# Performance work log

Measured on AMD Instinct MI355X. Metric: run time of the kernel, lower is better.

The kernel has to match this reference:

```python
import jax, jax.numpy as jnp
import numpy as np

K_MSG = 1024   # message length k (rows of G)
N_CODE = 2048  # codeword length n (cols of G)
B = 32768      # number of message blocks


def setup_inputs() -> dict:
    key = jax.random.key(0)
    kb, kg = jax.random.split(key)
    b = jax.random.randint(kb, (B, K_MSG), 0, 2, dtype=jnp.int32)
    G = jax.random.randint(kg, (K_MSG, N_CODE), 0, 2, dtype=jnp.int32)
    return {"b": b, "G": G}


def reference(b, G):
    # GF(2) linear block encode: c = (b @ G) mod 2
    # b: [num_blocks, k] bits (0/1), G: [k, n] generator matrix (0/1)
    b2 = b.astype(jnp.int32)
    G2 = G.astype(jnp.int32)
    c = jnp.mod(jnp.matmul(b2, G2), 2)  # [num_blocks, n]
    return c.astype(jnp.int32)
```

## Files before the change

kernel.cpp:

```cpp
#include <hip/hip_runtime.h>
#include <stdint.h>

typedef unsigned long long u64;
typedef unsigned int u32;
typedef u32 v4u __attribute__((ext_vector_type(4)));

#define K_MSG   1024
#define N_CODE  2048
#define NB      32768
#define KW      16
#define ROWS_TILE 256
#define COLS_PER_BLOCK 256

__global__ void pack_b_kernel(const int* __restrict__ b, u64* __restrict__ bp,
                              int nwords) {
    const int lane  = threadIdx.x & 63;
    const int wave  = blockIdx.x * (blockDim.x >> 6) + (threadIdx.x >> 6);
    const int nwave = gridDim.x * (blockDim.x >> 6);
    for (int word = wave; word < nwords; word += nwave) {
        int v = b[(size_t)word * 64 + lane];
        u64 m = __ballot((v & 1) != 0);
        if (lane == 0) bp[word] = m;
    }
}

__global__ void pack_g_kernel(const int* __restrict__ G, u64* __restrict__ gp) {
    const int lane = threadIdx.x & 63;
    const int wave = blockIdx.x * (blockDim.x >> 6) + (threadIdx.x >> 6);
    const int w    = wave >> 5;
    const int jb   = wave & 31;
    const int j    = jb * 64 + lane;
    u64 word = 0;
#pragma unroll 16
    for (int t = 0; t < 64; ++t) {
        int v = G[(size_t)(w * 64 + t) * N_CODE + j];
        word |= (u64)(v & 1) << t;
    }
    gp[(size_t)w * N_CODE + j] = word;
}

__global__ __launch_bounds__(256, 4) void encode_main(const u64* __restrict__ bp,
                                                      const u64* __restrict__ gp,
                                                      int* __restrict__ out) {
    __shared__ u32 rows[ROWS_TILE * 32];

    const int tid = threadIdx.x;
    const int j   = blockIdx.x * COLS_PER_BLOCK + tid;
    const int r0  = blockIdx.y * ROWS_TILE;

    u32 g[32];
#pragma unroll
    for (int w = 0; w < KW; ++w) {
        u64 v = gp[(size_t)w * N_CODE + j];
        g[2 * w]     = (u32)v;
        g[2 * w + 1] = (u32)(v >> 32);
    }

    {
        const v4u* __restrict__ src = (const v4u*)(bp + ((size_t)r0 << 4));
        v4u* dst = (v4u*)rows;
#pragma unroll
        for (int i = 0; i < 8; ++i)
            dst[tid + COLS_PER_BLOCK * i] = src[tid + COLS_PER_BLOCK * i];
    }
    __syncthreads();

    int* __restrict__ op = out + (size_t)r0 * N_CODE + j;

#pragma unroll 2
    for (int r = 0; r < ROWS_TILE; ++r) {
        const u32* rw = &rows[r * 32];
        u32 a0 = 0, a1 = 0, a2 = 0, a3 = 0;
#pragma unroll
        for (int i = 0; i < 8; ++i) {
            a0 ^= rw[i]      & g[i];
            a1 ^= rw[8 + i]  & g[8 + i];
            a2 ^= rw[16 + i] & g[16 + i];
            a3 ^= rw[24 + i] & g[24 + i];
        }
        u32 acc = (a0 ^ a1) ^ (a2 ^ a3);
        op[(size_t)r * N_CODE] = (int)(__popc(acc) & 1);
    }
}

__global__ void encode_naive(const int* __restrict__ b, const int* __restrict__ G,
                             int* __restrict__ out) {
    size_t idx = (size_t)blockIdx.x * blockDim.x + threadIdx.x;
    size_t total = (size_t)NB * N_CODE;
    if (idx >= total) return;
    int i = (int)(idx / N_CODE);
    int j = (int)(idx % N_CODE);
    int acc = 0;
    for (int k = 0; k < K_MSG; ++k)
        acc ^= b[(size_t)i * K_MSG + k] & G[(size_t)k * N_CODE + j];
    out[idx] = acc & 1;
}

extern "C" void kernel_launch(void* const* d_in, const int* in_sizes, int n_in,
                              void* d_out, int out_size, void* d_ws, size_t ws_size,
                              hipStream_t stream) {
    const int* b = (const int*)d_in[0];
    const int* G = (const int*)d_in[1];
    int* out = (int*)d_out;

    const size_t bp_bytes = (size_t)NB * KW * sizeof(u64);
    const size_t gp_bytes = (size_t)N_CODE * KW * sizeof(u64);

    if (ws_size < bp_bytes + gp_bytes) {
        size_t total = (size_t)NB * N_CODE;
        encode_naive<<<(unsigned)((total + 255) / 256), 256, 0, stream>>>(b, G, out);
        return;
    }

    u64* bp = (u64*)d_ws;
    u64* gp = (u64*)((char*)d_ws + bp_bytes);

    pack_b_kernel<<<2048, 256, 0, stream>>>(b, bp, NB * KW);
    pack_g_kernel<<<128, 256, 0, stream>>>(G, gp);

    dim3 grid(N_CODE / COLS_PER_BLOCK, NB / ROWS_TILE);
    encode_main<<<grid, 256, 0, stream>>>(bp, gp, out);
}
```

Measured before the change: 159.5 us.

## Replace bit-packed XOR/popcount encode with int8 MFMA GEMM

Replaces the 64-bit bit-packing and per-thread AND/XOR/popcount loop with an int8 GEMM on the matrix cores. The message matrix is packed to one byte per bit, and G is transposed to byte form. A double-buffered LDS-tiled kernel then accumulates with mfma_i32_32x32x32_i8 and takes the result mod 2. This moves the bulk arithmetic onto MFMA units, but the packed operands become 8x larger (32 MB for b instead of 4 MB), and the output stores from MFMA fragments are less coalesced.

```diff
diff --git a/kernel.cpp b/kernel.cpp
--- a/kernel.cpp
+++ b/kernel.cpp
@@ -1,85 +1,116 @@
 #include <hip/hip_runtime.h>
 #include <stdint.h>
 
-typedef unsigned long long u64;
 typedef unsigned int u32;
-typedef u32 v4u __attribute__((ext_vector_type(4)));
+typedef int v4i  __attribute__((ext_vector_type(4)));
+typedef int v16i __attribute__((ext_vector_type(16)));
 
 #define K_MSG   1024
 #define N_CODE  2048
 #define NB      32768
-#define KW      16
-#define ROWS_TILE 256
-#define COLS_PER_BLOCK 256
+#define BM 128
+#define BN 128
+#define BK 64
+#define BKP 80
 
-__global__ void pack_b_kernel(const int* __restrict__ b, u64* __restrict__ bp,
-                              int nwords) {
-    const int lane  = threadIdx.x & 63;
-    const int wave  = blockIdx.x * (blockDim.x >> 6) + (threadIdx.x >> 6);
-    const int nwave = gridDim.x * (blockDim.x >> 6);
-    for (int word = wave; word < nwords; word += nwave) {
-        int v = b[(size_t)word * 64 + lane];
-        u64 m = __ballot((v & 1) != 0);
-        if (lane == 0) bp[word] = m;
+__global__ void pack_bi8(const int* __restrict__ b, u32* __restrict__ bi8) {
+    const int nthr = gridDim.x * blockDim.x;
+    int idx = blockIdx.x * blockDim.x + threadIdx.x;
+    const int ndw = NB * K_MSG / 4;
+    for (; idx < ndw; idx += nthr) {
+        int4 v = *(const int4*)(b + (size_t)idx * 4);
+        bi8[idx] = (u32)(v.x & 1) | ((u32)(v.y & 1) << 8) |
+                   ((u32)(v.z & 1) << 16) | ((u32)(v.w & 1) << 24);
     }
 }
 
-__global__ void pack_g_kernel(const int* __restrict__ G, u64* __restrict__ gp) {
-    const int lane = threadIdx.x & 63;
-    const int wave = blockIdx.x * (blockDim.x >> 6) + (threadIdx.x >> 6);
-    const int w    = wave >> 5;
-    const int jb   = wave & 31;
-    const int j    = jb * 64 + lane;
-    u64 word = 0;
-#pragma unroll 16
-    for (int t = 0; t < 64; ++t) {
-        int v = G[(size_t)(w * 64 + t) * N_CODE + j];
-        word |= (u64)(v & 1) << t;
+__global__ void pack_gT8(const int* __restrict__ G, u32* __restrict__ gt8) {
+    int idx = blockIdx.x * blockDim.x + threadIdx.x;
+    const int j  = idx & (N_CODE - 1);
+    const int kq = idx >> 11;
+    u32 p = 0;
+#pragma unroll
+    for (int i = 0; i < 4; ++i) {
+        int v = G[(size_t)(kq * 4 + i) * N_CODE + j];
+        p |= (u32)(v & 1) << (8 * i);
     }
-    gp[(size_t)w * N_CODE + j] = word;
+    gt8[(size_t)j * (K_MSG / 4) + kq] = p;
 }
 
-__global__ __launch_bounds__(256, 4) void encode_main(const u64* __restrict__ bp,
-                                                      const u64* __restrict__ gp,
-                                                      int* __restrict__ out) {
-    __shared__ u32 rows[ROWS_TILE * 32];
+__global__ __launch_bounds__(256) void gemm_i8(const char* __restrict__ bi8,
+                                               const char* __restrict__ gt8,
+                                               int* __restrict__ out) {
+    __shared__ __align__(16) char As[2][BM][BKP];
+    __shared__ __align__(16) char Bs[2][BN][BKP];
 
-    const int tid = threadIdx.x;
-    const int j   = blockIdx.x * COLS_PER_BLOCK + tid;
-    const int r0  = blockIdx.y * ROWS_TILE;
+    const int t    = threadIdx.x;
+    const int m0   = blockIdx.y * BM;
+    const int n0   = blockIdx.x * BN;
+    const int srow = t & 127;
+    const int kh   = t >> 7;
+    const int w    = t >> 6, lane = t & 63, hi = lane >> 5, lr = lane & 31;
+    const int wm   = w >> 1, wn = w & 1;
 
-    u32 g[32];
-#pragma unroll
-    for (int w = 0; w < KW; ++w) {
-        u64 v = gp[(size_t)w * N_CODE + j];
-        g[2 * w]     = (u32)v;
-        g[2 * w + 1] = (u32)(v >> 32);
-    }
+    v16i acc[2][2] = {};
+
+    const char* aseg = bi8 + (size_t)(m0 + srow) * K_MSG + kh * 32;
+    const char* bseg = gt8 + (size_t)(n0 + srow) * K_MSG + kh * 32;
 
     {
-        const v4u* __restrict__ src = (const v4u*)(bp + ((size_t)r0 << 4));
-        v4u* dst = (v4u*)rows;
-#pragma unroll
-        for (int i = 0; i < 8; ++i)
-            dst[tid + COLS_PER_BLOCK * i] = src[tid + COLS_PER_BLOCK * i];
+        uint4 a0 = *(const uint4*)(aseg);
+        uint4 a1 = *(const uint4*)(aseg + 16);
+        uint4 b0 = *(const uint4*)(bseg);
+        uint4 b1 = *(const uint4*)(bseg + 16);
+        *(uint4*)&As[0][srow][kh * 32]      = a0;
+        *(uint4*)&As[0][srow][kh * 32 + 16] = a1;
+        *(uint4*)&Bs[0][srow][kh * 32]      = b0;
+        *(uint4*)&Bs[0][srow][kh * 32 + 16] = b1;
     }
     __syncthreads();
 
-    int* __restrict__ op = out + (size_t)r0 * N_CODE + j;
+    const int NSTEP = K_MSG / BK;
+#pragma unroll 1
+    for (int s = 0; s < NSTEP; ++s) {
+        const int cur = s & 1, nxt = cur ^ 1;
+        uint4 na0, na1, nb0, nb1;
+        if (s < NSTEP - 1) {
+            const char* ap = aseg + (size_t)(s + 1) * BK;
+            const char* bp = bseg + (size_t)(s + 1) * BK;
+            na0 = *(const uint4*)(ap);      na1 = *(const uint4*)(ap + 16);
+            nb0 = *(const uint4*)(bp);      nb1 = *(const uint4*)(bp + 16);
+        }
+#pragma unroll
+        for (int kc = 0; kc < 2; ++kc) {
+            v4i af0 = *(const v4i*)&As[cur][wm * 64 + lr]      [kc * 32 + hi * 16];
+            v4i af1 = *(const v4i*)&As[cur][wm * 64 + 32 + lr] [kc * 32 + hi * 16];
+            v4i bf0 = *(const v4i*)&Bs[cur][wn * 64 + lr]      [kc * 32 + hi * 16];
+            v4i bf1 = *(const v4i*)&Bs[cur][wn * 64 + 32 + lr] [kc * 32 + hi * 16];
+            acc[0][0] = __builtin_amdgcn_mfma_i32_32x32x32_i8(af0, bf0, acc[0][0], 0, 0, 0);
+            acc[0][1] = __builtin_amdgcn_mfma_i32_32x32x32_i8(af0, bf1, acc[0][1], 0, 0, 0);
+            acc[1][0] = __builtin_amdgcn_mfma_i32_32x32x32_i8(af1, bf0, acc[1][0], 0, 0, 0);
+            acc[1][1] = __builtin_amdgcn_mfma_i32_32x32x32_i8(af1, bf1, acc[1][1], 0, 0, 0);
+        }
+        if (s < NSTEP - 1) {
+            *(uint4*)&As[nxt][srow][kh * 32]      = na0;
+            *(uint4*)&As[nxt][srow][kh * 32 + 16] = na1;
+            *(uint4*)&Bs[nxt][srow][kh * 32]      = nb0;
+            *(uint4*)&Bs[nxt][srow][kh * 32 + 16] = nb1;
+        }
+        __syncthreads();
+    }
 
-#pragma unroll 2
-    for (int r = 0; r < ROWS_TILE; ++r) {
-        const u32* rw = &rows[r * 32];
-        u32 a0 = 0, a1 = 0, a2 = 0, a3 = 0;
 #pragma unroll
-        for (int i = 0; i < 8; ++i) {
-            a0 ^= rw[i]      & g[i];
-            a1 ^= rw[8 + i]  & g[8 + i];
-            a2 ^= rw[16 + i] & g[16 + i];
-            a3 ^= rw[24 + i] & g[24 + i];
+    for (int fm = 0; fm < 2; ++fm) {
+#pragma unroll
+        for (int fn = 0; fn < 2; ++fn) {
+            const int rbase = m0 + wm * 64 + fm * 32 + 4 * hi;
+            const int cbase = n0 + wn * 64 + fn * 32 + lr;
+#pragma unroll
+            for (int r = 0; r < 16; ++r) {
+                const int row = rbase + (r & 3) + 8 * (r >> 2);
+                out[(size_t)row * N_CODE + cbase] = acc[fm][fn][r] & 1;
+            }
         }
-        u32 acc = (a0 ^ a1) ^ (a2 ^ a3);
-        op[(size_t)r * N_CODE] = (int)(__popc(acc) & 1);
     }
 }
 
@@ -103,21 +134,21 @@
     const int* G = (const int*)d_in[1];
     int* out = (int*)d_out;
 
-    const size_t bp_bytes = (size_t)NB * KW * sizeof(u64);
-    const size_t gp_bytes = (size_t)N_CODE * KW * sizeof(u64);
+    const size_t bi8_bytes = (size_t)NB * K_MSG;
+    const size_t gt8_bytes = (size_t)N_CODE * K_MSG;
 
-    if (ws_size < bp_bytes + gp_bytes) {
+    if (ws_size < bi8_bytes + gt8_bytes) {
         size_t total = (size_t)NB * N_CODE;
         encode_naive<<<(unsigned)((total + 255) / 256), 256, 0, stream>>>(b, G, out);
         return;
     }
 
-    u64* bp = (u64*)d_ws;
-    u64* gp = (u64*)((char*)d_ws + bp_bytes);
+    char* bi8 = (char*)d_ws;
+    char* gt8 = (char*)d_ws + bi8_bytes;
 
-    pack_b_kernel<<<2048, 256, 0, stream>>>(b, bp, NB * KW);
-    pack_g_kernel<<<128, 256, 0, stream>>>(G, gp);
+    pack_bi8<<<2048, 256, 0, stream>>>(b, (u32*)bi8);
+    pack_gT8<<<2048, 256, 0, stream>>>(G, (u32*)gt8);
 
-    dim3 grid(N_CODE / COLS_PER_BLOCK, NB / ROWS_TILE);
-    encode_main<<<grid, 256, 0, stream>>>(bp, gp, out);
+    dim3 grid(N_CODE / BN, NB / BM);
+    gemm_i8<<<grid, 256, 0, stream>>>(bi8, gt8, out);
 }
```

Result: slower. 193.6 us (+21.4%).
